# Kernel optimization log

Hardware: AMD Instinct MI355X
Metric: run time of the kernel (lower is better)

The kernel has to match this reference:

```python
import jax, jax.numpy as jnp
import numpy as np

NNZ = 16777216  # 2**24 nonzeros
D = 2048        # dense size (D, D, D); sum over dim 2 -> (D, D)


def setup_inputs() -> dict:
    key = jax.random.key(0)
    kv, ki = jax.random.split(key)
    values = jax.random.normal(kv, (NNZ,), dtype=jnp.float32)
    indices = jax.random.randint(ki, (3, NNZ), 0, D, dtype=jnp.int64)
    return {"values": values, "indices": indices}


def reference(values, indices):
    # sparse_coo_tensor(indices, values, size=(D,D,D)) -> sparse.sum(dim=2) -> to_dense()
    # is equivalent to a scatter-add of values keyed by (indices[0], indices[1]):
    # the third index only distinguishes entries that get summed away, and COO
    # coalescing already sums duplicate coordinates.
    out = jnp.zeros((D, D), dtype=jnp.float32)
    out = out.at[indices[0], indices[1]].add(values)
    return out
```

## Files before the change

### kernel.cpp

```cpp
#include <hip/hip_runtime.h>

#define NNZ 16777216
#define D 2048
#define NB 512
#define ROWS_PER_B 4
#define CAP 35840u
#define K1_BLOCK 512
#define K1_EPT 16
#define K1_CHUNK (K1_BLOCK * K1_EPT)
#define K1_VEC (K1_EPT / 4)

__global__ void init_cursors(unsigned int* __restrict__ cursor) {
    int i = threadIdx.x;
    if (i < NB) cursor[i] = (unsigned int)i * CAP;
}

__global__ __launch_bounds__(K1_BLOCK) void bin_scatter(
    const float* __restrict__ values,
    const int* __restrict__ idx0,
    const int* __restrict__ idx1,
    unsigned int* __restrict__ bins,
    unsigned int* __restrict__ cursor)
{
    __shared__ unsigned int lhist[NB];
    __shared__ unsigned int sprefix[NB];
    __shared__ unsigned int sgbase[NB];
    __shared__ unsigned int wsum[8];
    __shared__ unsigned int skey[K1_CHUNK];
    __shared__ unsigned short sval[K1_CHUNK];

    const int tid = threadIdx.x;
    lhist[tid] = 0;
    __syncthreads();

    const int vecBase = blockIdx.x * (K1_CHUNK / 4);

    float4 v[K1_VEC]; int4 a[K1_VEC]; int4 c[K1_VEC];
#pragma unroll
    for (int it = 0; it < K1_VEC; ++it) {
        int g = vecBase + it * K1_BLOCK + tid;
        v[it] = reinterpret_cast<const float4*>(values)[g];
        a[it] = reinterpret_cast<const int4*>(idx0)[g];
        c[it] = reinterpret_cast<const int4*>(idx1)[g];
    }

    unsigned short rank[K1_EPT];
#pragma unroll
    for (int it = 0; it < K1_VEC; ++it) {
        const int* ap = reinterpret_cast<const int*>(&a[it]);
#pragma unroll
        for (int e = 0; e < 4; ++e)
            rank[it * 4 + e] = (unsigned short)atomicAdd(&lhist[ap[e] >> 2], 1u);
    }
    __syncthreads();

    {
        const int lane = tid & 63;
        const int wid = tid >> 6;
        unsigned int cnt = lhist[tid];
        unsigned int x = cnt;
#pragma unroll
        for (int dlt = 1; dlt < 64; dlt <<= 1) {
            unsigned int y = __shfl_up(x, dlt, 64);
            if (lane >= dlt) x += y;
        }
        if (lane == 63) wsum[wid] = x;
        sgbase[tid] = cnt ? atomicAdd(&cursor[tid], cnt) : 0u;
        __syncthreads();
        unsigned int off = 0;
#pragma unroll
        for (int wjj = 0; wjj < 8; ++wjj) off += (wjj < wid) ? wsum[wjj] : 0u;
        sprefix[tid] = x - cnt + off;
    }
    __syncthreads();

#pragma unroll
    for (int it = 0; it < K1_VEC; ++it) {
        const int*   ap = reinterpret_cast<const int*>(&a[it]);
        const int*   cp = reinterpret_cast<const int*>(&c[it]);
        const float* vp = reinterpret_cast<const float*>(&v[it]);
#pragma unroll
        for (int e = 0; e < 4; ++e) {
            int i0 = ap[e], i1 = cp[e];
            unsigned int slot = sprefix[i0 >> 2] + rank[it * 4 + e];
            unsigned int fb = __float_as_uint(vp[e]);
            skey[slot] = ((unsigned int)i0 << 11) | (unsigned int)i1;
            sval[slot] = (unsigned short)((fb + 0x7fffu + ((fb >> 16) & 1u)) >> 16);
        }
    }
    __syncthreads();

#pragma unroll
    for (int it = 0; it < K1_EPT; ++it) {
        int s = it * K1_BLOCK + tid;
        unsigned int k = skey[s];
        unsigned int b = k >> 13;
        unsigned int addr = sgbase[b] + ((unsigned int)s - sprefix[b]);
        if (addr < (b + 1) * CAP)
            bins[addr] = ((k & 0x1FFFu) << 16) | (unsigned int)sval[s];
    }
}

__global__ __launch_bounds__(1024) void bucket_accumulate(
    const unsigned int* __restrict__ bins,
    const unsigned int* __restrict__ cursor,
    float* __restrict__ out)
{
    __shared__ float tile[ROWS_PER_B * D];

    const int b = blockIdx.x;
    const int tid = threadIdx.x;

    for (int j = tid; j < ROWS_PER_B * D / 4; j += 1024)
        reinterpret_cast<float4*>(tile)[j] = make_float4(0.f, 0.f, 0.f, 0.f);
    __syncthreads();

    const unsigned int base = (unsigned int)b * CAP;
    unsigned int n = cursor[b] - base;
    if (n > CAP) n = CAP;

    const uint4* b4 = reinterpret_cast<const uint4*>(bins + base);
    const unsigned int nv = n >> 2;
    for (unsigned int i = tid; i < nv; i += 1024) {
        uint4 p = b4[i];
        atomicAdd(&tile[p.x >> 16], __uint_as_float(p.x << 16));
        atomicAdd(&tile[p.y >> 16], __uint_as_float(p.y << 16));
        atomicAdd(&tile[p.z >> 16], __uint_as_float(p.z << 16));
        atomicAdd(&tile[p.w >> 16], __uint_as_float(p.w << 16));
    }
    for (unsigned int i = (nv << 2) + tid; i < n; i += 1024) {
        unsigned int p = bins[base + i];
        atomicAdd(&tile[p >> 16], __uint_as_float(p << 16));
    }
    __syncthreads();

    float4* o4 = reinterpret_cast<float4*>(out + (size_t)b * ROWS_PER_B * D);
    for (int j = tid; j < ROWS_PER_B * D / 4; j += 1024)
        o4[j] = reinterpret_cast<float4*>(tile)[j];
}

__global__ __launch_bounds__(256) void scatter_add_kernel(
    const float* __restrict__ values,
    const int* __restrict__ idx0,
    const int* __restrict__ idx1,
    float* __restrict__ out)
{
    const int nvec = NNZ / 4;
    int tid = blockIdx.x * blockDim.x + threadIdx.x;
    int stride = gridDim.x * blockDim.x;
    for (int i = tid; i < nvec; i += stride) {
        const float4 v = reinterpret_cast<const float4*>(values)[i];
        const int4   a = reinterpret_cast<const int4*>(idx0)[i];
        const int4   b = reinterpret_cast<const int4*>(idx1)[i];
        atomicAdd(&out[a.x * D + b.x], v.x);
        atomicAdd(&out[a.y * D + b.y], v.y);
        atomicAdd(&out[a.z * D + b.z], v.z);
        atomicAdd(&out[a.w * D + b.w], v.w);
    }
}

extern "C" void kernel_launch(void* const* d_in, const int* in_sizes, int n_in,
                              void* d_out, int out_size, void* d_ws, size_t ws_size,
                              hipStream_t stream) {
    const float* values  = (const float*)d_in[0];
    const int*   indices = (const int*)d_in[1];
    const int*   idx0 = indices;
    const int*   idx1 = indices + NNZ;
    float* out = (float*)d_out;

    const size_t need = 4096 + (size_t)NB * CAP * sizeof(unsigned int);

    if (ws_size < need) {
        hipMemsetAsync(out, 0, (size_t)out_size * sizeof(float), stream);
        const int nvec = NNZ / 4;
        scatter_add_kernel<<<(nvec + 255) / 256, 256, 0, stream>>>(values, idx0, idx1, out);
        return;
    }

    unsigned int* cursor = (unsigned int*)d_ws;
    unsigned int* bins   = (unsigned int*)((char*)d_ws + 4096);

    init_cursors<<<1, NB, 0, stream>>>(cursor);
    bin_scatter<<<NNZ / K1_CHUNK, K1_BLOCK, 0, stream>>>(values, idx0, idx1, bins, cursor);
    bucket_accumulate<<<NB, 1024, 0, stream>>>(bins, cursor, out);
}
```

Before: 163.4 us.

## Retune binning and accumulate kernels, unroll bin loads, memset cursors

The binning kernel now uses 1024-thread blocks with 8 elements per thread, with the histogram and scan steps guarded to the first 512 threads. The accumulate kernel drops to 512 threads and issues eight independent 16-byte bin loads per iteration before its LDS atomics, aiming for more loads in flight. The cursor-init kernel is replaced by a memset, with cursors now relative offsets per bin. Risks are lower occupancy from the larger LDS-heavy blocks in the first kernel and higher register pressure in the unrolled loop.

```diff
diff --git a/kernel.cpp b/kernel.cpp
--- a/kernel.cpp
+++ b/kernel.cpp
@@ -5,17 +5,13 @@
 #define NB 512
 #define ROWS_PER_B 4
 #define CAP 35840u
-#define K1_BLOCK 512
-#define K1_EPT 16
+#define K1_BLOCK 1024
+#define K1_EPT 8
 #define K1_CHUNK (K1_BLOCK * K1_EPT)
 #define K1_VEC (K1_EPT / 4)
-
-__global__ void init_cursors(unsigned int* __restrict__ cursor) {
-    int i = threadIdx.x;
-    if (i < NB) cursor[i] = (unsigned int)i * CAP;
-}
-
-__global__ __launch_bounds__(K1_BLOCK) void bin_scatter(
+#define K2_BLOCK 512
+
+__global__ __launch_bounds__(K1_BLOCK, 8) void bin_scatter(
     const float* __restrict__ values,
     const int* __restrict__ idx0,
     const int* __restrict__ idx1,
@@ -30,7 +26,7 @@
     __shared__ unsigned short sval[K1_CHUNK];
 
     const int tid = threadIdx.x;
-    lhist[tid] = 0;
+    if (tid < NB) lhist[tid] = 0;
     __syncthreads();
 
     const int vecBase = blockIdx.x * (K1_CHUNK / 4);
@@ -54,19 +50,22 @@
     }
     __syncthreads();
 
-    {
+    unsigned int x = 0, cnt = 0;
+    if (tid < NB) {
         const int lane = tid & 63;
-        const int wid = tid >> 6;
-        unsigned int cnt = lhist[tid];
-        unsigned int x = cnt;
+        cnt = lhist[tid];
+        x = cnt;
 #pragma unroll
         for (int dlt = 1; dlt < 64; dlt <<= 1) {
             unsigned int y = __shfl_up(x, dlt, 64);
             if (lane >= dlt) x += y;
         }
-        if (lane == 63) wsum[wid] = x;
+        if (lane == 63) wsum[tid >> 6] = x;
         sgbase[tid] = cnt ? atomicAdd(&cursor[tid], cnt) : 0u;
-        __syncthreads();
+    }
+    __syncthreads();
+    if (tid < NB) {
+        const int wid = tid >> 6;
         unsigned int off = 0;
 #pragma unroll
         for (int wjj = 0; wjj < 8; ++wjj) off += (wjj < wid) ? wsum[wjj] : 0u;
@@ -95,13 +94,13 @@
         int s = it * K1_BLOCK + tid;
         unsigned int k = skey[s];
         unsigned int b = k >> 13;
-        unsigned int addr = sgbase[b] + ((unsigned int)s - sprefix[b]);
-        if (addr < (b + 1) * CAP)
-            bins[addr] = ((k & 0x1FFFu) << 16) | (unsigned int)sval[s];
-    }
-}
-
-__global__ __launch_bounds__(1024) void bucket_accumulate(
+        unsigned int rel = sgbase[b] + ((unsigned int)s - sprefix[b]);
+        if (rel < CAP)
+            bins[b * CAP + rel] = ((k & 0x1FFFu) << 16) | (unsigned int)sval[s];
+    }
+}
+
+__global__ __launch_bounds__(K2_BLOCK, 8) void bucket_accumulate(
     const unsigned int* __restrict__ bins,
     const unsigned int* __restrict__ cursor,
     float* __restrict__ out)
@@ -111,31 +110,75 @@
     const int b = blockIdx.x;
     const int tid = threadIdx.x;
 
-    for (int j = tid; j < ROWS_PER_B * D / 4; j += 1024)
+    for (int j = tid; j < ROWS_PER_B * D / 4; j += K2_BLOCK)
         reinterpret_cast<float4*>(tile)[j] = make_float4(0.f, 0.f, 0.f, 0.f);
     __syncthreads();
 
+    unsigned int n = cursor[b];
+    if (n > CAP) n = CAP;
     const unsigned int base = (unsigned int)b * CAP;
-    unsigned int n = cursor[b] - base;
-    if (n > CAP) n = CAP;
 
     const uint4* b4 = reinterpret_cast<const uint4*>(bins + base);
     const unsigned int nv = n >> 2;
-    for (unsigned int i = tid; i < nv; i += 1024) {
+
+    unsigned int i = tid;
+    for (; i + 7u * K2_BLOCK < nv; i += 8u * K2_BLOCK) {
+        uint4 p0 = b4[i];
+        uint4 p1 = b4[i + 1u * K2_BLOCK];
+        uint4 p2 = b4[i + 2u * K2_BLOCK];
+        uint4 p3 = b4[i + 3u * K2_BLOCK];
+        uint4 p4 = b4[i + 4u * K2_BLOCK];
+        uint4 p5 = b4[i + 5u * K2_BLOCK];
+        uint4 p6 = b4[i + 6u * K2_BLOCK];
+        uint4 p7 = b4[i + 7u * K2_BLOCK];
+        atomicAdd(&tile[p0.x >> 16], __uint_as_float(p0.x << 16));
+        atomicAdd(&tile[p0.y >> 16], __uint_as_float(p0.y << 16));
+        atomicAdd(&tile[p0.z >> 16], __uint_as_float(p0.z << 16));
+        atomicAdd(&tile[p0.w >> 16], __uint_as_float(p0.w << 16));
+        atomicAdd(&tile[p1.x >> 16], __uint_as_float(p1.x << 16));
+        atomicAdd(&tile[p1.y >> 16], __uint_as_float(p1.y << 16));
+        atomicAdd(&tile[p1.z >> 16], __uint_as_float(p1.z << 16));
+        atomicAdd(&tile[p1.w >> 16], __uint_as_float(p1.w << 16));
+        atomicAdd(&tile[p2.x >> 16], __uint_as_float(p2.x << 16));
+        atomicAdd(&tile[p2.y >> 16], __uint_as_float(p2.y << 16));
+        atomicAdd(&tile[p2.z >> 16], __uint_as_float(p2.z << 16));
+        atomicAdd(&tile[p2.w >> 16], __uint_as_float(p2.w << 16));
+        atomicAdd(&tile[p3.x >> 16], __uint_as_float(p3.x << 16));
+        atomicAdd(&tile[p3.y >> 16], __uint_as_float(p3.y << 16));
+        atomicAdd(&tile[p3.z >> 16], __uint_as_float(p3.z << 16));
+        atomicAdd(&tile[p3.w >> 16], __uint_as_float(p3.w << 16));
+        atomicAdd(&tile[p4.x >> 16], __uint_as_float(p4.x << 16));
+        atomicAdd(&tile[p4.y >> 16], __uint_as_float(p4.y << 16));
+        atomicAdd(&tile[p4.z >> 16], __uint_as_float(p4.z << 16));
+        atomicAdd(&tile[p4.w >> 16], __uint_as_float(p4.w << 16));
+        atomicAdd(&tile[p5.x >> 16], __uint_as_float(p5.x << 16));
+        atomicAdd(&tile[p5.y >> 16], __uint_as_float(p5.y << 16));
+        atomicAdd(&tile[p5.z >> 16], __uint_as_float(p5.z << 16));
+        atomicAdd(&tile[p5.w >> 16], __uint_as_float(p5.w << 16));
+        atomicAdd(&tile[p6.x >> 16], __uint_as_float(p6.x << 16));
+        atomicAdd(&tile[p6.y >> 16], __uint_as_float(p6.y << 16));
+        atomicAdd(&tile[p6.z >> 16], __uint_as_float(p6.z << 16));
+        atomicAdd(&tile[p6.w >> 16], __uint_as_float(p6.w << 16));
+        atomicAdd(&tile[p7.x >> 16], __uint_as_float(p7.x << 16));
+        atomicAdd(&tile[p7.y >> 16], __uint_as_float(p7.y << 16));
+        atomicAdd(&tile[p7.z >> 16], __uint_as_float(p7.z << 16));
+        atomicAdd(&tile[p7.w >> 16], __uint_as_float(p7.w << 16));
+    }
+    for (; i < nv; i += K2_BLOCK) {
         uint4 p = b4[i];
         atomicAdd(&tile[p.x >> 16], __uint_as_float(p.x << 16));
         atomicAdd(&tile[p.y >> 16], __uint_as_float(p.y << 16));
         atomicAdd(&tile[p.z >> 16], __uint_as_float(p.z << 16));
         atomicAdd(&tile[p.w >> 16], __uint_as_float(p.w << 16));
     }
-    for (unsigned int i = (nv << 2) + tid; i < n; i += 1024) {
-        unsigned int p = bins[base + i];
+    for (unsigned int s = (nv << 2) + tid; s < n; s += K2_BLOCK) {
+        unsigned int p = bins[base + s];
         atomicAdd(&tile[p >> 16], __uint_as_float(p << 16));
     }
     __syncthreads();
 
     float4* o4 = reinterpret_cast<float4*>(out + (size_t)b * ROWS_PER_B * D);
-    for (int j = tid; j < ROWS_PER_B * D / 4; j += 1024)
+    for (int j = tid; j < ROWS_PER_B * D / 4; j += K2_BLOCK)
         o4[j] = reinterpret_cast<float4*>(tile)[j];
 }
 
@@ -180,7 +223,7 @@
     unsigned int* cursor = (unsigned int*)d_ws;
     unsigned int* bins   = (unsigned int*)((char*)d_ws + 4096);
 
-    init_cursors<<<1, NB, 0, stream>>>(cursor);
+    hipMemsetAsync(cursor, 0, NB * sizeof(unsigned int), stream);
     bin_scatter<<<NNZ / K1_CHUNK, K1_BLOCK, 0, stream>>>(values, idx0, idx1, bins, cursor);
-    bucket_accumulate<<<NB, 1024, 0, stream>>>(bins, cursor, out);
-}
+    bucket_accumulate<<<NB, K2_BLOCK, 0, stream>>>(bins, cursor, out);
+}
```

Result: no change. 164.8 us (+0.9%).
